# Performance work log

Hardware: AMD Instinct MI355X
Metric: run time of the kernel (lower is better)

The kernel has to match this reference:

```python
import jax, jax.numpy as jnp
import numpy as np
from jax import lax

BS, L, HID = 16, 512, 768
H, HD, NREG = 12, 64, 8
R2 = 2 * NREG


def setup_inputs() -> dict:
    key = jax.random.key(0)
    ks = jax.random.split(key, 7)
    s = 1.0 / np.sqrt(HID)
    return {
        "hidden_states": jax.random.normal(ks[0], (BS, L, HID), jnp.float32),
        "K1_w": jax.random.normal(ks[1], (H * HD, HID), jnp.float32) * s,
        "K1_b": jnp.zeros((H * HD,), jnp.float32),
        "V1_w": jax.random.normal(ks[2], (H * HD, HID), jnp.float32) * s,
        "V1_b": jnp.zeros((H * HD,), jnp.float32),
        "reading_head": jax.random.normal(ks[3], (H, HD), jnp.float32) * (1.0 / np.sqrt(HD)),
        "bidirection_weight": jnp.ones((1, 1, H, 1, R2), jnp.float32) * (1.0 / R2),
    }


def _softmax_dim1(x):
    # torch: softmax over length dim (1) plus 1/exp(max) residual term
    m = jnp.max(x, axis=1, keepdims=True)
    e = jnp.exp(x - m)
    return e / jnp.sum(e, axis=1, keepdims=True) + jnp.exp(-m)


def _cummax_idx(e):
    # torch.cummax indices over axis=1 for a bool tensor (ties -> latest index):
    # last True index so far; if no True yet, current index.
    ar = jnp.arange(e.shape[1], dtype=jnp.int32)[None, :, None]
    lt = lax.cummax(jnp.where(e, ar, jnp.int32(-1)), axis=1)
    return jnp.where(lt >= 0, lt, ar)


def reference(hidden_states, K1_w, K1_b, V1_w, V1_b, reading_head, bidirection_weight):
    bs, length, _ = hidden_states.shape
    K1 = jax.nn.relu(hidden_states @ K1_w.T + K1_b).reshape(bs, length, H, HD)
    V1 = jax.nn.relu(hidden_states @ V1_w.T + V1_b).reshape(bs, length, H, HD)

    scores = jnp.einsum("blhn,hn->blh", K1, reading_head)
    events = _softmax_dim1(scores) > (1.5 / length)  # (bs, L, H) bool; fwd==bwd for IC1

    col0 = _cummax_idx(events)  # (bs, L, H)
    rolled = jnp.roll(events, -1, axis=1)
    col1 = jnp.flip(512 - _cummax_idx(jnp.flip(rolled, axis=1)), axis=1)
    col1 = col1.at[:, 0].set(0)

    # sequential shift-register scan over length
    e_seq = jnp.moveaxis(events, 1, 0)  # (L, bs, H)
    f_seq = jnp.moveaxis(col0, 1, 0)
    b_seq = jnp.moveaxis(col1, 1, 0)
    row0 = jnp.concatenate(
        [f_seq[0][:, None], b_seq[0][:, None], jnp.zeros((bs, R2, H), jnp.int32)], axis=1
    )  # (bs, R2+2, H)

    def step(row, inp):
        e, f, b = inp
        reg = jnp.where(e[:, None, :], row[:, :-2], row[:, 2:])  # shift-in on event
        new_row = jnp.concatenate([f[:, None], b[:, None], reg], axis=1)
        return new_row, reg

    _, regs = lax.scan(step, row0, (e_seq[1:], f_seq[1:], b_seq[1:]))
    regs = jnp.concatenate([jnp.zeros((1, bs, R2, H), jnp.int32), regs], axis=0)  # (L,bs,R2,H)
    idx = jnp.moveaxis(regs, 0, 1).reshape(bs, length * R2, H)
    idx = jnp.clip(idx, 0, length - 1)

    V2 = jnp.take_along_axis(V1, idx[..., None], axis=1).reshape(bs, length, R2, H, HD)
    w = bidirection_weight.reshape(H, R2)
    return jnp.einsum("blrhd,hr->blhd", V2, w)  # (bs, L, H, HD)
```

## Files before the change

### kernel.cpp

```cpp
#include <hip/hip_runtime.h>
#include <cstdint>
#include <cstddef>

#define BSZ 16
#define LQ  512
#define HIDDIM 768
#define NH  12
#define HD  64
#define R2V 16
#define NTOT 1536
#define MTOT 8192

typedef __bf16 bf16x8 __attribute__((ext_vector_type(8)));
typedef float  f32x4  __attribute__((ext_vector_type(4)));

__device__ inline unsigned short f2bf(float x) {
    union { float f; unsigned u; } c; c.f = x;
    unsigned r = c.u + 0x7fffu + ((c.u >> 16) & 1u);
    return (unsigned short)(r >> 16);
}
__device__ inline float bfl(unsigned u) { return __uint_as_float(u << 16); }
__device__ inline float bfh(unsigned u) { return __uint_as_float(u & 0xffff0000u); }

#define NHS4 1572864
#define NW1  147456
#define NW4  294912

__global__ __launch_bounds__(256) void cast_pack(
    const float* __restrict__ hs,
    const float* __restrict__ Kw, const float* __restrict__ Vw,
    const float* __restrict__ Kb, const float* __restrict__ Vb,
    unsigned short* __restrict__ hsb, unsigned short* __restrict__ Wb,
    float* __restrict__ biasp)
{
    const int i = blockIdx.x * 256 + threadIdx.x;
    float4 v; unsigned short* dst;
    if (i < NHS4) {
        v = ((const float4*)hs)[i];
        dst = hsb + (size_t)i * 4;
    } else {
        const int j = i - NHS4;
        v = (j < NW1) ? ((const float4*)Kw)[j] : ((const float4*)Vw)[j - NW1];
        dst = Wb + (size_t)j * 4;
    }
    ushort4 o;
    o.x = f2bf(v.x); o.y = f2bf(v.y); o.z = f2bf(v.z); o.w = f2bf(v.w);
    *(ushort4*)dst = o;
    if (i < 768) { biasp[i] = Kb[i]; biasp[768 + i] = Vb[i]; }
}

#define TBM 256
#define TBN 256
#define TBK 32
#define KT  (HIDDIM / TBK)
#define ATILE (TBM * TBK)

#define GLD16(g, l) __builtin_amdgcn_global_load_lds( \
    (const __attribute__((address_space(1))) void*)(g), \
    (__attribute__((address_space(3))) void*)(l), 16, 0, 0)

__global__ __launch_bounds__(512, 2) void gemm_mfma(
    const unsigned short* __restrict__ Abf,
    const unsigned short* __restrict__ Wbf,
    const float* __restrict__ biasp,
    unsigned short* __restrict__ K1b, unsigned short* __restrict__ V1b)
{
    __shared__ unsigned short As[2][ATILE];
    __shared__ unsigned short Bs[2][ATILE];

    const int n0   = blockIdx.x * TBN;
    const int m0   = blockIdx.y * TBM;
    const int tid  = threadIdx.x;
    const int wid  = tid >> 6;
    const int lane = tid & 63;
    const int wr   = wid >> 2;
    const int wc   = wid & 3;

    f32x4 acc[8][4] = {};

    const int srow = lane >> 2;
    const int scol = ((lane & 3) ^ ((lane >> 3) & 3)) << 3;
    const int r0   = wid * 32;

    const unsigned short* Ag = Abf + (size_t)(m0 + r0 + srow) * HIDDIM + scol;
    const unsigned short* Bg = Wbf + (size_t)(n0 + r0 + srow) * HIDDIM + scol;

#define STAGE(buf, kt) do {                                                   \
        const int kof_ = (kt) * TBK;                                          \
        GLD16(Ag + kof_,                    &As[buf][r0 * TBK]);              \
        GLD16(Ag + 16 * HIDDIM + kof_,      &As[buf][(r0 + 16) * TBK]);       \
        GLD16(Bg + kof_,                    &Bs[buf][r0 * TBK]);              \
        GLD16(Bg + 16 * HIDDIM + kof_,      &Bs[buf][(r0 + 16) * TBK]);       \
    } while (0)

    const int fm   = lane & 15;
    const int fj   = lane >> 4;
    const int koff = ((fj ^ ((fm >> 1) & 3)) << 3);

    STAGE(0, 0);

    for (int kt = 0; kt < KT; ++kt) {
        __syncthreads();
        if (kt + 1 < KT) STAGE((kt + 1) & 1, kt + 1);
        const int cb = kt & 1;

        bf16x8 af[8], bfr[4];
        #pragma unroll
        for (int mi = 0; mi < 8; ++mi)
            af[mi] = *reinterpret_cast<const bf16x8*>(
                &As[cb][(wr * 128 + mi * 16 + fm) * TBK + koff]);
        #pragma unroll
        for (int ni = 0; ni < 4; ++ni)
            bfr[ni] = *reinterpret_cast<const bf16x8*>(
                &Bs[cb][(wc * 64 + ni * 16 + fm) * TBK + koff]);
        __builtin_amdgcn_s_setprio(1);
        #pragma unroll
        for (int mi = 0; mi < 8; ++mi)
            #pragma unroll
            for (int ni = 0; ni < 4; ++ni)
                acc[mi][ni] = __builtin_amdgcn_mfma_f32_16x16x32_bf16(
                    bfr[ni], af[mi], acc[mi][ni], 0, 0, 0);
        __builtin_amdgcn_s_setprio(0);
    }
#undef STAGE

    const bool isK = (n0 < HIDDIM);
    unsigned short* __restrict__ dst = isK ? K1b : V1b;
    const int nsub = isK ? 0 : HIDDIM;
    const int nq   = fj * 4;

    #pragma unroll
    for (int ni = 0; ni < 4; ++ni) {
        const int ng = n0 + wc * 64 + ni * 16 + nq;
        const float4 bv = *(const float4*)(biasp + ng);
        #pragma unroll
        for (int mi = 0; mi < 8; ++mi) {
            const int mg = m0 + wr * 128 + mi * 16 + fm;
            f32x4 a = acc[mi][ni];
            ushort4 o;
            o.x = f2bf(fmaxf(a[0] + bv.x, 0.f));
            o.y = f2bf(fmaxf(a[1] + bv.y, 0.f));
            o.z = f2bf(fmaxf(a[2] + bv.z, 0.f));
            o.w = f2bf(fmaxf(a[3] + bv.w, 0.f));
            *(ushort4*)(dst + (size_t)mg * HIDDIM + (ng - nsub)) = o;
        }
    }
}

#define SINF (1 << 30)
#define IXP 17

__global__ __launch_bounds__(512) void scan_gather(
    const unsigned short* __restrict__ K1b,
    const unsigned short* __restrict__ V1b,
    const float* __restrict__ rh,
    const float* __restrict__ bw,
    float* __restrict__ out)
{
    const int bh   = blockIdx.x >> 2;
    const int part = blockIdx.x & 3;
    const int b    = bh / NH;
    const int h    = bh % NH;
    const int l    = threadIdx.x;
    const int lane = l & 63;
    const int wid  = l >> 6;

    __shared__ float wredA[8];
    __shared__ float wredB[8];
    __shared__ int   wp0[8];
    __shared__ int   wp1[8];
    __shared__ int   wp2[8];
    __shared__ int   ev[LQ];
    __shared__ int   col0[LQ];
    __shared__ int   col1[LQ];
    __shared__ int   E[LQ];
    __shared__ int   idxs[LQ * IXP];
    __shared__ float wsm[R2V];

    if (l < R2V) wsm[l] = bw[h * R2V + l];

    const unsigned short* krow = K1b + ((size_t)(b * LQ + l)) * HIDDIM + h * HD;
    const float* rrow = rh + h * HD;
    float s = 0.f;
    #pragma unroll
    for (int c8 = 0; c8 < 8; ++c8) {
        uint4 kv = *(const uint4*)(krow + c8 * 8);
        float4 ra = *(const float4*)(rrow + c8 * 8);
        float4 rb = *(const float4*)(rrow + c8 * 8 + 4);
        s += bfl(kv.x) * ra.x + bfh(kv.x) * ra.y
           + bfl(kv.y) * ra.z + bfh(kv.y) * ra.w
           + bfl(kv.z) * rb.x + bfh(kv.z) * rb.y
           + bfl(kv.w) * rb.z + bfh(kv.w) * rb.w;
    }

    float mx = s;
    #pragma unroll
    for (int off = 32; off > 0; off >>= 1) mx = fmaxf(mx, __shfl_xor(mx, off));
    if (lane == 0) wredA[wid] = mx;
    __syncthreads();
    float m = wredA[0];
    #pragma unroll
    for (int i = 1; i < 8; ++i) m = fmaxf(m, wredA[i]);

    const float e = expf(s - m);
    float sm = e;
    #pragma unroll
    for (int off = 32; off > 0; off >>= 1) sm += __shfl_xor(sm, off);
    if (lane == 0) wredB[wid] = sm;
    __syncthreads();
    float ssum = 0.f;
    #pragma unroll
    for (int i = 0; i < 8; ++i) ssum += wredB[i];

    const float p = e / ssum + expf(-m);
    const int event = (p > (1.5f / 512.0f)) ? 1 : 0;
    ev[l] = event;

    int v = event ? l : -1;
    #pragma unroll
    for (int off = 1; off < 64; off <<= 1) {
        int u = __shfl_up(v, off);
        if (lane >= off) v = (u > v) ? u : v;
    }
    if (lane == 63) wp0[wid] = v;
    __syncthreads();
    int pfx = -1;
    for (int i = 0; i < wid; ++i) pfx = (wp0[i] > pfx) ? wp0[i] : pfx;
    v = (pfx > v) ? pfx : v;
    col0[l] = (v >= 0) ? v : l;

    int v1 = ev[(l + 1) & (LQ - 1)] ? l : SINF;
    #pragma unroll
    for (int off = 1; off < 64; off <<= 1) {
        int u = __shfl_down(v1, off);
        if (lane < 64 - off) v1 = (u < v1) ? u : v1;
    }
    if (lane == 0) wp1[wid] = v1;
    __syncthreads();
    int sfx = SINF;
    for (int i = wid + 1; i < 8; ++i) sfx = (wp1[i] < sfx) ? wp1[i] : sfx;
    v1 = (sfx < v1) ? sfx : v1;
    col1[l] = (l == 0) ? 0 : (((v1 < SINF) ? v1 : l) + 1);

    int c = (l >= 1) ? event : 0;
    #pragma unroll
    for (int off = 1; off < 64; off <<= 1) {
        int u = __shfl_up(c, off);
        if (lane >= off) c += u;
    }
    if (lane == 63) wp2[wid] = c;
    __syncthreads();
    for (int i = 0; i < wid; ++i) c += wp2[i];

    if (l >= 1 && event) E[c - 1] = l;
    __syncthreads();

    int* op = &idxs[l * IXP];
    #pragma unroll
    for (int j = 0; j < 8; ++j) {
        const int k = c - 1 - j;
        int f = 0, bb = 0;
        if (k >= 0) {
            const int t = E[k];
            f  = col0[t - 1];
            bb = col1[t - 1];
        }
        op[2 * j]     = min(max(f, 0), LQ - 1);
        op[2 * j + 1] = min(max(bb, 0), LQ - 1);
    }
    __syncthreads();

    const int dsl = lane & 7;
    const size_t vbase = (size_t)b * LQ * HIDDIM + h * HD + dsl * 8;

    for (int rr = 0; rr < 2; ++rr) {
        const int round = part * 2 + rr;
        const int lg = round * 64 + wid * 8 + (lane >> 3);
        const int* ip = &idxs[lg * IXP];
        float a0 = 0.f, a1 = 0.f, a2 = 0.f, a3 = 0.f;
        float a4 = 0.f, a5 = 0.f, a6 = 0.f, a7 = 0.f;
        #pragma unroll 1
        for (int rc = 0; rc < R2V; rc += 4) {
            const int i0 = ip[rc], i1 = ip[rc + 1], i2 = ip[rc + 2], i3 = ip[rc + 3];
            uint4 v0 = *(const uint4*)(V1b + vbase + (size_t)i0 * HIDDIM);
            uint4 vA = *(const uint4*)(V1b + vbase + (size_t)i1 * HIDDIM);
            uint4 vB = *(const uint4*)(V1b + vbase + (size_t)i2 * HIDDIM);
            uint4 vC = *(const uint4*)(V1b + vbase + (size_t)i3 * HIDDIM);
            const float w0 = wsm[rc], w1 = wsm[rc + 1], w2 = wsm[rc + 2], w3 = wsm[rc + 3];
            a0 += w0 * bfl(v0.x); a1 += w0 * bfh(v0.x);
            a2 += w0 * bfl(v0.y); a3 += w0 * bfh(v0.y);
            a4 += w0 * bfl(v0.z); a5 += w0 * bfh(v0.z);
            a6 += w0 * bfl(v0.w); a7 += w0 * bfh(v0.w);
            a0 += w1 * bfl(vA.x); a1 += w1 * bfh(vA.x);
            a2 += w1 * bfl(vA.y); a3 += w1 * bfh(vA.y);
            a4 += w1 * bfl(vA.z); a5 += w1 * bfh(vA.z);
            a6 += w1 * bfl(vA.w); a7 += w1 * bfh(vA.w);
            a0 += w2 * bfl(vB.x); a1 += w2 * bfh(vB.x);
            a2 += w2 * bfl(vB.y); a3 += w2 * bfh(vB.y);
            a4 += w2 * bfl(vB.z); a5 += w2 * bfh(vB.z);
            a6 += w2 * bfl(vB.w); a7 += w2 * bfh(vB.w);
            a0 += w3 * bfl(vC.x); a1 += w3 * bfh(vC.x);
            a2 += w3 * bfl(vC.y); a3 += w3 * bfh(vC.y);
            a4 += w3 * bfl(vC.z); a5 += w3 * bfh(vC.z);
            a6 += w3 * bfl(vC.w); a7 += w3 * bfh(vC.w);
        }
        float* po = out + ((size_t)(b * LQ + lg) * NH + h) * HD + dsl * 8;
        *(float4*)po       = make_float4(a0, a1, a2, a3);
        *((float4*)po + 1) = make_float4(a4, a5, a6, a7);
    }
}

extern "C" void kernel_launch(void* const* d_in, const int* in_sizes, int n_in,
                              void* d_out, int out_size, void* d_ws, size_t ws_size,
                              hipStream_t stream)
{
    (void)in_sizes; (void)n_in; (void)out_size; (void)ws_size;

    const float* hs = (const float*)d_in[0];
    const float* Kw = (const float*)d_in[1];
    const float* Kb = (const float*)d_in[2];
    const float* Vw = (const float*)d_in[3];
    const float* Vb = (const float*)d_in[4];
    const float* rh = (const float*)d_in[5];
    const float* bw = (const float*)d_in[6];
    float* out = (float*)d_out;

    char* ws = (char*)d_ws;
    unsigned short* K1b   = (unsigned short*)(ws);
    unsigned short* V1b   = (unsigned short*)(ws + 12582912);
    unsigned short* hsb   = (unsigned short*)(ws + 25165824);
    unsigned short* Wb    = (unsigned short*)(ws + 37748736);
    float*          biasp = (float*)(ws + 40108032);

    cast_pack<<<(NHS4 + NW4) / 256, 256, 0, stream>>>(hs, Kw, Vw, Kb, Vb, hsb, Wb, biasp);

    dim3 g1(NTOT / TBN, MTOT / TBM);
    gemm_mfma<<<g1, 512, 0, stream>>>(hsb, Wb, biasp, K1b, V1b);

    scan_gather<<<BSZ * NH * 4, LQ, 0, stream>>>(K1b, V1b, rh, bw, out);
}
```

Before: 152.4 us.

## Shrink GEMM tiles to 128x128 with triple-buffered LDS and XCD-aware block swizzle

Reworks the bf16 MFMA projection GEMM to use 128x128 tiles with 256 threads (4 waves of 64x64), giving 768 workgroups instead of 192 so the 256 CUs fill better. The shared-memory staging moves from double to triple buffering with explicit vmcnt waits and raw barriers, so the next loads can be in flight while the current tile is computed. Workgroup ids are remapped so neighbouring tiles land on the same XCD for L2 reuse. Smaller tiles mean each loaded element is reused less, and the hand-written waitcnt logic must match the load count to stay correct.

Result: faster. 141.0 us (median of 2 runs) (-7.5%).

```diff
diff --git a/kernel.cpp b/kernel.cpp
--- a/kernel.cpp
+++ b/kernel.cpp
@@ -49,8 +49,8 @@
     if (i < 768) { biasp[i] = Kb[i]; biasp[768 + i] = Vb[i]; }
 }
 
-#define TBM 256
-#define TBN 256
+#define TBM 128
+#define TBN 128
 #define TBK 32
 #define KT  (HIDDIM / TBK)
 #define ATILE (TBM * TBK)
@@ -59,24 +59,29 @@
     (const __attribute__((address_space(1))) void*)(g), \
     (__attribute__((address_space(3))) void*)(l), 16, 0, 0)
 
-__global__ __launch_bounds__(512, 2) void gemm_mfma(
+__global__ __launch_bounds__(256, 3) void gemm_mfma(
     const unsigned short* __restrict__ Abf,
     const unsigned short* __restrict__ Wbf,
     const float* __restrict__ biasp,
     unsigned short* __restrict__ K1b, unsigned short* __restrict__ V1b)
 {
-    __shared__ unsigned short As[2][ATILE];
-    __shared__ unsigned short Bs[2][ATILE];
-
-    const int n0   = blockIdx.x * TBN;
-    const int m0   = blockIdx.y * TBM;
+    __shared__ unsigned short As[3][ATILE];
+    __shared__ unsigned short Bs[3][ATILE];
+
+    const int wg  = blockIdx.y * 12 + blockIdx.x;
+    const int nid = (wg & 7) * 96 + (wg >> 3);
+    const int bx  = nid % 12;
+    const int by  = nid / 12;
+    const int n0  = bx * TBN;
+    const int m0  = by * TBM;
+
     const int tid  = threadIdx.x;
     const int wid  = tid >> 6;
     const int lane = tid & 63;
-    const int wr   = wid >> 2;
-    const int wc   = wid & 3;
-
-    f32x4 acc[8][4] = {};
+    const int wm   = (wid & 1) * 64;
+    const int wn   = (wid >> 1) * 64;
+
+    f32x4 acc[4][4] = {};
 
     const int srow = lane >> 2;
     const int scol = ((lane & 3) ^ ((lane >> 3) & 3)) << 3;
@@ -87,10 +92,10 @@
 
 #define STAGE(buf, kt) do {                                                   \
         const int kof_ = (kt) * TBK;                                          \
-        GLD16(Ag + kof_,                    &As[buf][r0 * TBK]);              \
-        GLD16(Ag + 16 * HIDDIM + kof_,      &As[buf][(r0 + 16) * TBK]);       \
-        GLD16(Bg + kof_,                    &Bs[buf][r0 * TBK]);              \
-        GLD16(Bg + 16 * HIDDIM + kof_,      &Bs[buf][(r0 + 16) * TBK]);       \
+        GLD16(Ag + kof_,               &As[buf][r0 * TBK]);                   \
+        GLD16(Ag + 16 * HIDDIM + kof_, &As[buf][(r0 + 16) * TBK]);            \
+        GLD16(Bg + kof_,               &Bs[buf][r0 * TBK]);                   \
+        GLD16(Bg + 16 * HIDDIM + kof_, &Bs[buf][(r0 + 16) * TBK]);            \
     } while (0)
 
     const int fm   = lane & 15;
@@ -98,24 +103,28 @@
     const int koff = ((fj ^ ((fm >> 1) & 3)) << 3);
 
     STAGE(0, 0);
+    STAGE(1, 1);
 
     for (int kt = 0; kt < KT; ++kt) {
-        __syncthreads();
-        if (kt + 1 < KT) STAGE((kt + 1) & 1, kt + 1);
-        const int cb = kt & 1;
-
-        bf16x8 af[8], bfr[4];
+        if (kt < KT - 1) asm volatile("s_waitcnt vmcnt(4)" ::: "memory");
+        else             asm volatile("s_waitcnt vmcnt(0)" ::: "memory");
+        __builtin_amdgcn_s_barrier();
+        __builtin_amdgcn_sched_barrier(0);
+        if (kt + 2 < KT) STAGE((kt + 2) % 3, kt + 2);
+        const int cb = kt % 3;
+
+        bf16x8 af[4], bfr[4];
         #pragma unroll
-        for (int mi = 0; mi < 8; ++mi)
+        for (int mi = 0; mi < 4; ++mi)
             af[mi] = *reinterpret_cast<const bf16x8*>(
-                &As[cb][(wr * 128 + mi * 16 + fm) * TBK + koff]);
+                &As[cb][(wm + mi * 16 + fm) * TBK + koff]);
         #pragma unroll
         for (int ni = 0; ni < 4; ++ni)
             bfr[ni] = *reinterpret_cast<const bf16x8*>(
-                &Bs[cb][(wc * 64 + ni * 16 + fm) * TBK + koff]);
+                &Bs[cb][(wn + ni * 16 + fm) * TBK + koff]);
         __builtin_amdgcn_s_setprio(1);
         #pragma unroll
-        for (int mi = 0; mi < 8; ++mi)
+        for (int mi = 0; mi < 4; ++mi)
             #pragma unroll
             for (int ni = 0; ni < 4; ++ni)
                 acc[mi][ni] = __builtin_amdgcn_mfma_f32_16x16x32_bf16(
@@ -130,12 +139,12 @@
     const int nq   = fj * 4;
 
     #pragma unroll
-    for (int ni = 0; ni < 4; ++ni) {
-        const int ng = n0 + wc * 64 + ni * 16 + nq;
-        const float4 bv = *(const float4*)(biasp + ng);
+    for (int mi = 0; mi < 4; ++mi) {
+        const int mg = m0 + wm + mi * 16 + fm;
         #pragma unroll
-        for (int mi = 0; mi < 8; ++mi) {
-            const int mg = m0 + wr * 128 + mi * 16 + fm;
+        for (int ni = 0; ni < 4; ++ni) {
+            const int ng = n0 + wn + ni * 16 + nq;
+            float4 bv = *(const float4*)(biasp + ng);
             f32x4 a = acc[mi][ni];
             ushort4 o;
             o.x = f2bf(fmaxf(a[0] + bv.x, 0.f));
@@ -335,7 +344,7 @@
     cast_pack<<<(NHS4 + NW4) / 256, 256, 0, stream>>>(hs, Kw, Vw, Kb, Vb, hsb, Wb, biasp);
 
     dim3 g1(NTOT / TBN, MTOT / TBM);
-    gemm_mfma<<<g1, 512, 0, stream>>>(hsb, Wb, biasp, K1b, V1b);
+    gemm_mfma<<<g1, 256, 0, stream>>>(hsb, Wb, biasp, K1b, V1b);
 
     scan_gather<<<BSZ * NH * 4, LQ, 0, stream>>>(K1b, V1b, rh, bw, out);
 }
```
